# Optimization experiments

Measured on AMD Instinct MI355X. Metric: run time of the kernel, lower is better.

The kernel has to match this reference:

```python
import jax, jax.numpy as jnp
import numpy as np

N, E, G = 50000, 800000, 64
DIN, HID, OUT, ED = 128, 64, 96, 32
BN_EPS = 1e-5


def setup_inputs() -> dict:
    key = jax.random.key(0)
    ks = jax.random.split(key, 40)
    d = {}
    d["x"] = jax.random.normal(ks[0], (N, DIN), dtype=jnp.float32)
    d["edge_attr"] = jax.random.normal(ks[1], (E, ED), dtype=jnp.float32)
    d["edge_index"] = jax.random.randint(ks[2], (2, E), 0, N)
    d["batch"] = jnp.sort(jax.random.randint(ks[3], (N,), 0, G))
    dims = [(DIN, HID), (HID, HID), (HID, OUT)]  # (layer input dim, layer output dim)
    i = 4
    for l, (din, dout) in enumerate(dims):
        d[f"le{l}_w"] = jax.random.normal(ks[i], (ED, din), dtype=jnp.float32) * 0.05; i += 1
        d[f"le{l}_b"] = jnp.zeros((din,), dtype=jnp.float32)
        d[f"m{l}_w1"] = jax.random.normal(ks[i], (din, dout), dtype=jnp.float32) * 0.05; i += 1
        d[f"m{l}_b1"] = jnp.zeros((dout,), dtype=jnp.float32)
        d[f"m{l}_w2"] = jax.random.normal(ks[i], (dout, dout), dtype=jnp.float32) * 0.05; i += 1
        d[f"m{l}_b2"] = jnp.zeros((dout,), dtype=jnp.float32)
        d[f"bn{l}_g"] = jnp.ones((dout,), dtype=jnp.float32)
        d[f"bn{l}_b"] = jnp.zeros((dout,), dtype=jnp.float32)
        d[f"bn{l}_m"] = jax.random.normal(ks[i], (dout,), dtype=jnp.float32) * 0.01; i += 1
        d[f"bn{l}_v"] = jnp.ones((dout,), dtype=jnp.float32) + jax.random.uniform(ks[i], (dout,), dtype=jnp.float32) * 0.1; i += 1
    return d


def _gine_layer(x, src, dst, edge_attr, lew, leb, w1, b1, w2, b2,
                bng, bnb, bnm, bnv):
    # GINEConv: message = relu(x_j + Lin(edge_attr)); aggregate = sum into dst
    e = edge_attr @ lew + leb                      # [E, din]
    m = jax.nn.relu(x[src] + e)                    # [E, din]
    agg = jax.ops.segment_sum(m, dst, num_segments=x.shape[0])
    h = x + agg                                    # (1 + eps) * x + agg, eps = 0
    h = jax.nn.relu(h @ w1 + b1) @ w2 + b2         # 2-layer MLP
    # BatchNorm1d (eval: running stats) then ReLU; dropout is identity in eval
    h = (h - bnm) * (bng * jax.lax.rsqrt(bnv + BN_EPS)) + bnb
    return jax.nn.relu(h)


def reference(x, edge_attr,
              le0_w, le0_b, m0_w1, m0_b1, m0_w2, m0_b2, bn0_g, bn0_b, bn0_m, bn0_v,
              le1_w, le1_b, m1_w1, m1_b1, m1_w2, m1_b2, bn1_g, bn1_b, bn1_m, bn1_v,
              le2_w, le2_b, m2_w1, m2_b1, m2_w2, m2_b2, bn2_g, bn2_b, bn2_m, bn2_v,
              edge_index, batch):
    src, dst = edge_index[0], edge_index[1]
    h = _gine_layer(x, src, dst, edge_attr, le0_w, le0_b, m0_w1, m0_b1, m0_w2, m0_b2,
                    bn0_g, bn0_b, bn0_m, bn0_v)
    h = _gine_layer(h, src, dst, edge_attr, le1_w, le1_b, m1_w1, m1_b1, m1_w2, m1_b2,
                    bn1_g, bn1_b, bn1_m, bn1_v)
    h = _gine_layer(h, src, dst, edge_attr, le2_w, le2_b, m2_w1, m2_b1, m2_w2, m2_b2,
                    bn2_g, bn2_b, bn2_m, bn2_v)
    # global mean pool over graphs
    sums = jax.ops.segment_sum(h, batch, num_segments=G)            # [G, OUT]
    cnts = jax.ops.segment_sum(jnp.ones((h.shape[0],), h.dtype), batch, num_segments=G)
    return sums / jnp.maximum(cnts, 1.0)[:, None]
```

## Files before the change

kernel.cpp:

```cpp
#include <hip/hip_runtime.h>
#include <hip/hip_bf16.h>

#define N_NODES 50000
#define N_EDGES 800000
#define N_GRAPHS 64

__global__ __launch_bounds__(256) void hist_kernel(const int* __restrict__ ei,
                                                   int* __restrict__ deg, int E) {
  int e = blockIdx.x * 256 + threadIdx.x;
  if (e < E) atomicAdd(&deg[ei[E + e]], 1);
}

__global__ __launch_bounds__(1024) void scan_kernel(const int* __restrict__ deg,
                                                    int* __restrict__ row_start,
                                                    int* __restrict__ cursor, int N) {
  __shared__ int part[1024];
  const int t = threadIdx.x;
  const int C = (N + 1023) / 1024;
  const int b0 = min(t * C, N);
  const int b1 = min(b0 + C, N);
  int s = 0;
  for (int i = b0; i < b1; ++i) s += deg[i];
  part[t] = s;
  __syncthreads();
  for (int off = 1; off < 1024; off <<= 1) {
    int v = (t >= off) ? part[t - off] : 0;
    __syncthreads();
    part[t] += v;
    __syncthreads();
  }
  int ex = (t == 0) ? 0 : part[t - 1];
  for (int i = b0; i < b1; ++i) {
    row_start[i] = ex;
    cursor[i] = ex;
    ex += deg[i];
  }
  if (t == 1023) row_start[N] = part[1023];
}

__global__ __launch_bounds__(256) void scatter_kernel(const int* __restrict__ ei,
                                                      int* __restrict__ cursor,
                                                      int2* __restrict__ epair, int E) {
  int e = blockIdx.x * 256 + threadIdx.x;
  if (e < E) {
    int d = ei[E + e];
    int p = atomicAdd(&cursor[d], 1);
    epair[p] = make_int2(e, ei[e]);
  }
}

template <int DIN>
__global__ __launch_bounds__(256) void gine_gather(
    const float* __restrict__ x, const float* __restrict__ ea,
    const int* __restrict__ row_start, const int2* __restrict__ epair,
    const float* __restrict__ lew, const float* __restrict__ leb,
    float* __restrict__ hpre, int N) {
  constexpr int WPN = DIN / 64;
  __shared__ float wlds[32 * DIN];
  const int tid = threadIdx.x;
  for (int i = tid; i < 32 * DIN / 4; i += 256)
    ((float4*)wlds)[i] = ((const float4*)lew)[i];
  __syncthreads();

  const int gw = blockIdx.x * 4 + (tid >> 6);
  if (gw >= N * WPN) return;
  const int lane = tid & 63;
  const int n = gw / WPN;
  const int off = (gw % WPN) * 64 + lane;

  const float bb = leb[off];
  const int e0 = row_start[n];
  const int e1 = row_start[n + 1];
  float acc = 0.f;

  for (int i = e0; i < e1; i += 4) {
    int ee[4], ss[4];
    float val[4];
#pragma unroll
    for (int j = 0; j < 4; ++j) {
      const int idx = (i + j < e1) ? (i + j) : (e1 - 1);
      const int2 p = epair[idx];
      ee[j] = __builtin_amdgcn_readfirstlane(p.x);
      ss[j] = __builtin_amdgcn_readfirstlane(p.y);
      val[j] = (i + j < e1) ? 1.f : 0.f;
    }
    float xv[4], t[4];
#pragma unroll
    for (int j = 0; j < 4; ++j) {
      xv[j] = x[(size_t)ss[j] * DIN + off];
      t[j] = bb;
    }
    const float* __restrict__ r0 = ea + (size_t)ee[0] * 32;
    const float* __restrict__ r1 = ea + (size_t)ee[1] * 32;
    const float* __restrict__ r2 = ea + (size_t)ee[2] * 32;
    const float* __restrict__ r3 = ea + (size_t)ee[3] * 32;
#pragma unroll
    for (int k = 0; k < 32; ++k) {
      const float wk = wlds[k * DIN + off];
      t[0] = fmaf(r0[k], wk, t[0]);
      t[1] = fmaf(r1[k], wk, t[1]);
      t[2] = fmaf(r2[k], wk, t[2]);
      t[3] = fmaf(r3[k], wk, t[3]);
    }
#pragma unroll
    for (int j = 0; j < 4; ++j) acc += val[j] * fmaxf(xv[j] + t[j], 0.f);
  }
  hpre[(size_t)n * DIN + off] = x[(size_t)n * DIN + off] + acc;
}

template <int K, int M>
__global__ __launch_bounds__((M / 4) * 8) void mlp_fused(
    const float* __restrict__ in, const float* __restrict__ w1,
    const float* __restrict__ b1, const float* __restrict__ w2,
    const float* __restrict__ b2, const float* __restrict__ bng,
    const float* __restrict__ bnb, const float* __restrict__ bnm,
    const float* __restrict__ bnv, float* __restrict__ out, int N) {
  constexpr int NPB = 32;
  constexpr int SK = K + 4;
  constexpr int SH = M + 4;
  constexpr int Q = M / 4;
  constexpr int TH = Q * 8;
  constexpr int R1 = K * M + NPB * SK;
  constexpr int SZA = (R1 > M * M) ? R1 : (M * M);
  __shared__ alignas(16) float smem[SZA + NPB * SH + 2 * M];
  float* w1l = smem;
  float* hin = smem + K * M;
  float* w2l = smem;
  float* h1 = smem + SZA;
  float* bnA = h1 + NPB * SH;
  float* bnB = bnA + M;

  const int tid = threadIdx.x;
  const int nb = blockIdx.x * NPB;

  for (int i = tid; i < K * M / 4; i += TH)
    ((float4*)w1l)[i] = ((const float4*)w1)[i];
  for (int f = tid; f < M; f += TH) {
    const float s = bng[f] * rsqrtf(bnv[f] + 1e-5f);
    bnA[f] = s;
    bnB[f] = bnb[f] - bnm[f] * s;
  }
  for (int i = tid; i < NPB * (K / 4); i += TH) {
    const int dn = i / (K / 4);
    const int kq = i % (K / 4);
    const int n = nb + dn;
    float4 v = make_float4(0.f, 0.f, 0.f, 0.f);
    if (n < N) v = ((const float4*)(in + (size_t)n * K))[kq];
    ((float4*)(hin + dn * SK))[kq] = v;
  }
  __syncthreads();

  const int q = tid % Q;
  const int ng = tid / Q;

  {
    const float4 bias = ((const float4*)b1)[q];
    float4 a[4] = {bias, bias, bias, bias};
#pragma unroll 4
    for (int k = 0; k < K; ++k) {
      const float4 wv = ((const float4*)w1l)[k * Q + q];
#pragma unroll
      for (int r = 0; r < 4; ++r) {
        const float hv = hin[(ng * 4 + r) * SK + k];
        a[r].x = fmaf(hv, wv.x, a[r].x);
        a[r].y = fmaf(hv, wv.y, a[r].y);
        a[r].z = fmaf(hv, wv.z, a[r].z);
        a[r].w = fmaf(hv, wv.w, a[r].w);
      }
    }
    __syncthreads();
#pragma unroll
    for (int r = 0; r < 4; ++r) {
      float4 v = a[r];
      v.x = fmaxf(v.x, 0.f);
      v.y = fmaxf(v.y, 0.f);
      v.z = fmaxf(v.z, 0.f);
      v.w = fmaxf(v.w, 0.f);
      ((float4*)(h1 + (ng * 4 + r) * SH))[q] = v;
    }
  }
  for (int i = tid; i < M * M / 4; i += TH)
    ((float4*)w2l)[i] = ((const float4*)w2)[i];
  __syncthreads();

  {
    const float4 bias = ((const float4*)b2)[q];
    float4 a[4] = {bias, bias, bias, bias};
#pragma unroll 4
    for (int k = 0; k < M; ++k) {
      const float4 wv = ((const float4*)w2l)[k * Q + q];
#pragma unroll
      for (int r = 0; r < 4; ++r) {
        const float hv = h1[(ng * 4 + r) * SH + k];
        a[r].x = fmaf(hv, wv.x, a[r].x);
        a[r].y = fmaf(hv, wv.y, a[r].y);
        a[r].z = fmaf(hv, wv.z, a[r].z);
        a[r].w = fmaf(hv, wv.w, a[r].w);
      }
    }
    const float4 A = ((const float4*)bnA)[q];
    const float4 B = ((const float4*)bnB)[q];
#pragma unroll
    for (int r = 0; r < 4; ++r) {
      const int n = nb + ng * 4 + r;
      if (n < N) {
        float4 v = a[r];
        v.x = fmaxf(fmaf(v.x, A.x, B.x), 0.f);
        v.y = fmaxf(fmaf(v.y, A.y, B.y), 0.f);
        v.z = fmaxf(fmaf(v.z, A.z, B.z), 0.f);
        v.w = fmaxf(fmaf(v.w, A.w, B.w), 0.f);
        ((float4*)(out + (size_t)n * M))[q] = v;
      }
    }
  }
}

__global__ __launch_bounds__(128) void pool_kernel(const float* __restrict__ h,
                                                   const int* __restrict__ batch,
                                                   float* __restrict__ sums,
                                                   int* __restrict__ cnt, int N) {
  const int f = threadIdx.x;
  const int chunk = (N + gridDim.x - 1) / gridDim.x;
  const int n0 = blockIdx.x * chunk;
  const int n1 = min(n0 + chunk, N);
  int curg = -1;
  float acc = 0.f;
  int c = 0;
  for (int n = n0; n < n1; ++n) {
    const int g = batch[n];
    if (g != curg) {
      if (curg >= 0) {
        if (f < 96) unsafeAtomicAdd(&sums[curg * 96 + f], acc);
        if (f == 0) atomicAdd(&cnt[curg], c);
      }
      curg = g;
      acc = 0.f;
      c = 0;
    }
    if (f < 96) acc += h[(size_t)n * 96 + f];
    ++c;
  }
  if (curg >= 0) {
    if (f < 96) unsafeAtomicAdd(&sums[curg * 96 + f], acc);
    if (f == 0) atomicAdd(&cnt[curg], c);
  }
}

__global__ void finalize_kernel(const float* __restrict__ sums,
                                const int* __restrict__ cnt, float* __restrict__ out) {
  const int i = blockIdx.x * blockDim.x + threadIdx.x;
  if (i < N_GRAPHS * 96) {
    const int g = i / 96;
    const float c = (float)cnt[g];
    out[i] = sums[i] / fmaxf(c, 1.f);
  }
}

extern "C" void kernel_launch(void* const* d_in, const int* in_sizes, int n_in,
                              void* d_out, int out_size, void* d_ws, size_t ws_size,
                              hipStream_t stream) {
  const int N = N_NODES;
  const int E = N_EDGES;

  const float* x = (const float*)d_in[0];
  const float* ea = (const float*)d_in[1];
  const int* ei = (const int*)d_in[2];
  const int* batch = (const int*)d_in[3];
  auto L = [&](int l, int idx) { return (const float*)d_in[4 + 10 * l + idx]; };

  int* iws = (int*)d_ws;
  int* deg = iws;
  int* row_start = deg + N;
  int* cursor = row_start + N + 1;
  int2* epair = (int2*)(iws + 150004);
  float* fws = (float*)(iws + 150004 + 2 * E);
  float* hpre = fws;
  float* hA = hpre + (size_t)N * 128;
  float* hB = hA + (size_t)N * 96;
  float* sums = hB + (size_t)N * 64;
  int* cnt = (int*)(sums + N_GRAPHS * 96);

  const int gE = (E + 255) / 256;
  const int gN32 = (N + 31) / 32;

  hipMemsetAsync(deg, 0, (size_t)N * 4, stream);
  hist_kernel<<<gE, 256, 0, stream>>>(ei, deg, E);
  scan_kernel<<<1, 1024, 0, stream>>>(deg, row_start, cursor, N);
  scatter_kernel<<<gE, 256, 0, stream>>>(ei, cursor, epair, E);

  gine_gather<128><<<(N * 2 + 3) / 4, 256, 0, stream>>>(
      x, ea, row_start, epair, L(0, 0), L(0, 1), hpre, N);
  mlp_fused<128, 64><<<gN32, 128, 0, stream>>>(
      hpre, L(0, 2), L(0, 3), L(0, 4), L(0, 5), L(0, 6), L(0, 7), L(0, 8), L(0, 9), hA, N);

  gine_gather<64><<<(N + 3) / 4, 256, 0, stream>>>(
      hA, ea, row_start, epair, L(1, 0), L(1, 1), hpre, N);
  mlp_fused<64, 64><<<gN32, 128, 0, stream>>>(
      hpre, L(1, 2), L(1, 3), L(1, 4), L(1, 5), L(1, 6), L(1, 7), L(1, 8), L(1, 9), hB, N);

  gine_gather<64><<<(N + 3) / 4, 256, 0, stream>>>(
      hB, ea, row_start, epair, L(2, 0), L(2, 1), hpre, N);
  mlp_fused<64, 96><<<gN32, 192, 0, stream>>>(
      hpre, L(2, 2), L(2, 3), L(2, 4), L(2, 5), L(2, 6), L(2, 7), L(2, 8), L(2, 9), hA, N);

  hipMemsetAsync(sums, 0, (size_t)(N_GRAPHS * 96 + N_GRAPHS) * 4, stream);
  pool_kernel<<<512, 128, 0, stream>>>(hA, batch, sums, cnt, N);
  finalize_kernel<<<48, 128, 0, stream>>>(sums, cnt, (float*)d_out);
}
```

Baseline: 975.0 us.

## Process whole node per wavefront and software-pipeline edge gathers in GINE aggregation

The gather kernel now assigns one wavefront per node, and each lane handles DIN/64 features, so for DIN=128 the edge-attribute row and index loads are shared across both halves instead of being repeated by two wavefronts. The edge-weight matrix is permuted in LDS so each lane reads its features as a float2. Edge indices and source-node features for the next group of four edges are prefetched while the current group is computed, to hide gather latency. The cost is higher register pressure from the double-buffered state, and half as many wavefronts for layer 0.

Result: slower. 1.405 ms (+44.1%).

```diff
diff --git a/kernel.cpp b/kernel.cpp
--- a/kernel.cpp
+++ b/kernel.cpp
@@ -55,57 +55,106 @@
     const int* __restrict__ row_start, const int2* __restrict__ epair,
     const float* __restrict__ lew, const float* __restrict__ leb,
     float* __restrict__ hpre, int N) {
-  constexpr int WPN = DIN / 64;
+  constexpr int FPL = DIN / 64;
   __shared__ float wlds[32 * DIN];
   const int tid = threadIdx.x;
-  for (int i = tid; i < 32 * DIN / 4; i += 256)
-    ((float4*)wlds)[i] = ((const float4*)lew)[i];
+  for (int i = tid; i < 32 * DIN; i += 256) {
+    const int k = i / DIN;
+    const int c = i - k * DIN;
+    const int l = c / FPL;
+    const int p = c - l * FPL;
+    wlds[i] = lew[k * DIN + p * 64 + l];
+  }
   __syncthreads();
 
-  const int gw = blockIdx.x * 4 + (tid >> 6);
-  if (gw >= N * WPN) return;
+  const int n = blockIdx.x * 4 + (tid >> 6);
+  if (n >= N) return;
   const int lane = tid & 63;
-  const int n = gw / WPN;
-  const int off = (gw % WPN) * 64 + lane;
-
-  const float bb = leb[off];
+
+  float bb[FPL], acc[FPL];
+#pragma unroll
+  for (int p = 0; p < FPL; ++p) {
+    bb[p] = leb[p * 64 + lane];
+    acc[p] = 0.f;
+  }
   const int e0 = row_start[n];
   const int e1 = row_start[n + 1];
-  float acc = 0.f;
-
-  for (int i = e0; i < e1; i += 4) {
-    int ee[4], ss[4];
-    float val[4];
-#pragma unroll
-    for (int j = 0; j < 4; ++j) {
-      const int idx = (i + j < e1) ? (i + j) : (e1 - 1);
-      const int2 p = epair[idx];
-      ee[j] = __builtin_amdgcn_readfirstlane(p.x);
-      ss[j] = __builtin_amdgcn_readfirstlane(p.y);
-      val[j] = (i + j < e1) ? 1.f : 0.f;
-    }
-    float xv[4], t[4];
-#pragma unroll
-    for (int j = 0; j < 4; ++j) {
-      xv[j] = x[(size_t)ss[j] * DIN + off];
-      t[j] = bb;
-    }
-    const float* __restrict__ r0 = ea + (size_t)ee[0] * 32;
-    const float* __restrict__ r1 = ea + (size_t)ee[1] * 32;
-    const float* __restrict__ r2 = ea + (size_t)ee[2] * 32;
-    const float* __restrict__ r3 = ea + (size_t)ee[3] * 32;
-#pragma unroll
-    for (int k = 0; k < 32; ++k) {
-      const float wk = wlds[k * DIN + off];
-      t[0] = fmaf(r0[k], wk, t[0]);
-      t[1] = fmaf(r1[k], wk, t[1]);
-      t[2] = fmaf(r2[k], wk, t[2]);
-      t[3] = fmaf(r3[k], wk, t[3]);
-    }
-#pragma unroll
-    for (int j = 0; j < 4; ++j) acc += val[j] * fmaxf(xv[j] + t[j], 0.f);
-  }
-  hpre[(size_t)n * DIN + off] = x[(size_t)n * DIN + off] + acc;
+
+  if (e1 > e0) {
+    int ce[4], cs[4];
+    float cm[4], cx[4][FPL];
+    auto LOADM = [&](int i, int* e_, int* s_, float* m_, float (*x_)[FPL]) {
+#pragma unroll
+      for (int j = 0; j < 4; ++j) {
+        const int idx = (i + j < e1) ? (i + j) : (e1 - 1);
+        const int2 pr = epair[idx];
+        e_[j] = __builtin_amdgcn_readfirstlane(pr.x);
+        s_[j] = __builtin_amdgcn_readfirstlane(pr.y);
+        m_[j] = (i + j < e1) ? 1.f : 0.f;
+      }
+#pragma unroll
+      for (int j = 0; j < 4; ++j)
+#pragma unroll
+        for (int p = 0; p < FPL; ++p)
+          x_[j][p] = x[(size_t)s_[j] * DIN + p * 64 + lane];
+    };
+
+    LOADM(e0, ce, cs, cm, cx);
+    for (int i = e0; i < e1; i += 4) {
+      int ne[4], ns_[4];
+      float nm[4], nx[4][FPL];
+      if (i + 4 < e1) LOADM(i + 4, ne, ns_, nm, nx);
+
+      const float* __restrict__ r0 = ea + (size_t)ce[0] * 32;
+      const float* __restrict__ r1 = ea + (size_t)ce[1] * 32;
+      const float* __restrict__ r2 = ea + (size_t)ce[2] * 32;
+      const float* __restrict__ r3 = ea + (size_t)ce[3] * 32;
+
+      float t[4][FPL];
+#pragma unroll
+      for (int j = 0; j < 4; ++j)
+#pragma unroll
+        for (int p = 0; p < FPL; ++p) t[j][p] = bb[p];
+
+#pragma unroll
+      for (int k = 0; k < 32; ++k) {
+        float wk[FPL];
+        if constexpr (FPL == 2) {
+          const float2 wv = *(const float2*)&wlds[k * DIN + 2 * lane];
+          wk[0] = wv.x;
+          wk[1] = wv.y;
+        } else {
+          wk[0] = wlds[k * 64 + lane];
+        }
+        const float a0 = r0[k], a1 = r1[k], a2 = r2[k], a3 = r3[k];
+#pragma unroll
+        for (int p = 0; p < FPL; ++p) {
+          t[0][p] = fmaf(a0, wk[p], t[0][p]);
+          t[1][p] = fmaf(a1, wk[p], t[1][p]);
+          t[2][p] = fmaf(a2, wk[p], t[2][p]);
+          t[3][p] = fmaf(a3, wk[p], t[3][p]);
+        }
+      }
+#pragma unroll
+      for (int j = 0; j < 4; ++j)
+#pragma unroll
+        for (int p = 0; p < FPL; ++p)
+          acc[p] += cm[j] * fmaxf(cx[j][p] + t[j][p], 0.f);
+
+#pragma unroll
+      for (int j = 0; j < 4; ++j) {
+        ce[j] = ne[j];
+        cs[j] = ns_[j];
+        cm[j] = nm[j];
+#pragma unroll
+        for (int p = 0; p < FPL; ++p) cx[j][p] = nx[j][p];
+      }
+    }
+  }
+#pragma unroll
+  for (int p = 0; p < FPL; ++p)
+    hpre[(size_t)n * DIN + p * 64 + lane] =
+        x[(size_t)n * DIN + p * 64 + lane] + acc[p];
 }
 
 template <int K, int M>
@@ -281,6 +330,7 @@
   int* cnt = (int*)(sums + N_GRAPHS * 96);
 
   const int gE = (E + 255) / 256;
+  const int gW = (N + 3) / 4;
   const int gN32 = (N + 31) / 32;
 
   hipMemsetAsync(deg, 0, (size_t)N * 4, stream);
@@ -288,17 +338,17 @@
   scan_kernel<<<1, 1024, 0, stream>>>(deg, row_start, cursor, N);
   scatter_kernel<<<gE, 256, 0, stream>>>(ei, cursor, epair, E);
 
-  gine_gather<128><<<(N * 2 + 3) / 4, 256, 0, stream>>>(
+  gine_gather<128><<<gW, 256, 0, stream>>>(
       x, ea, row_start, epair, L(0, 0), L(0, 1), hpre, N);
   mlp_fused<128, 64><<<gN32, 128, 0, stream>>>(
       hpre, L(0, 2), L(0, 3), L(0, 4), L(0, 5), L(0, 6), L(0, 7), L(0, 8), L(0, 9), hA, N);
 
-  gine_gather<64><<<(N + 3) / 4, 256, 0, stream>>>(
+  gine_gather<64><<<gW, 256, 0, stream>>>(
       hA, ea, row_start, epair, L(1, 0), L(1, 1), hpre, N);
   mlp_fused<64, 64><<<gN32, 128, 0, stream>>>(
       hpre, L(1, 2), L(1, 3), L(1, 4), L(1, 5), L(1, 6), L(1, 7), L(1, 8), L(1, 9), hB, N);
 
-  gine_gather<64><<<(N + 3) / 4, 256, 0, stream>>>(
+  gine_gather<64><<<gW, 256, 0, stream>>>(
       hB, ea, row_start, epair, L(2, 0), L(2, 1), hpre, N);
   mlp_fused<64, 96><<<gN32, 192, 0, stream>>>(
       hpre, L(2, 2), L(2, 3), L(2, 4), L(2, 5), L(2, 6), L(2, 7), L(2, 8), L(2, 9), hA, N);
```
